# Kernel tuning notes

Measured on AMD Instinct MI355X. Metric: run time of the kernel, lower is better.

The kernel has to match this reference:

```python
import jax, jax.numpy as jnp
import numpy as np

VOCAB, EMBED, HIDDEN = 256, 512, 1024
B, T = 64, 512


def setup_inputs() -> dict:
    key = jax.random.key(0)
    ks = jax.random.split(key, 12)
    s = 0.02
    return {
        "x": jax.random.randint(ks[0], (B, T), 0, VOCAB),
        "embed": jax.random.normal(ks[1], (VOCAB, EMBED), jnp.float32) * s,
        "Wih0": jax.random.normal(ks[2], (3 * HIDDEN, EMBED), jnp.float32) * s,
        "Whh0": jax.random.normal(ks[3], (3 * HIDDEN, HIDDEN), jnp.float32) * s,
        "bih0": jax.random.normal(ks[4], (3 * HIDDEN,), jnp.float32) * s,
        "bhh0": jax.random.normal(ks[5], (3 * HIDDEN,), jnp.float32) * s,
        "Wih1": jax.random.normal(ks[6], (3 * HIDDEN, HIDDEN), jnp.float32) * s,
        "Whh1": jax.random.normal(ks[7], (3 * HIDDEN, HIDDEN), jnp.float32) * s,
        "bih1": jax.random.normal(ks[8], (3 * HIDDEN,), jnp.float32) * s,
        "bhh1": jax.random.normal(ks[9], (3 * HIDDEN,), jnp.float32) * s,
        "W_out": jax.random.normal(ks[10], (VOCAB, HIDDEN), jnp.float32) * s,
        "b_out": jax.random.normal(ks[11], (VOCAB,), jnp.float32) * s,
    }


def gru_cell(inp, h, Wih, Whh, bih, bhh):
    # PyTorch GRUCell math.
    gi = inp @ Wih.T + bih  # (B, 3H)
    gh = h @ Whh.T + bhh    # (B, 3H)
    i_r, i_z, i_n = jnp.split(gi, 3, axis=-1)
    h_r, h_z, h_n = jnp.split(gh, 3, axis=-1)
    r = jax.nn.sigmoid(i_r + h_r)
    z = jax.nn.sigmoid(i_z + h_z)
    n = jnp.tanh(i_n + r * h_n)
    return (1.0 - z) * n + z * h


def reference(x, embed, Wih0, Whh0, bih0, bhh0, Wih1, Whh1, bih1, bhh1, W_out, b_out):
    emb = embed[x]                       # (B, T, E)
    xs = jnp.swapaxes(emb, 0, 1)         # (T, B, E)
    h0 = jnp.zeros((x.shape[0], HIDDEN), emb.dtype)

    def step(carry, inp_t):
        h_0, h_1 = carry
        h_0 = gru_cell(inp_t, h_0, Wih0, Whh0, bih0, bhh0)
        h_1 = gru_cell(h_0, h_1, Wih1, Whh1, bih1, bhh1)
        return (h_0, h_1), h_1

    _, outs = jax.lax.scan(step, (h0, h0), xs)   # outs: (T, B, H)
    outs = jnp.swapaxes(outs, 0, 1)              # (B, T, H)
    logits = outs @ W_out.T + b_out              # (B, T, V)
    return logits
```

## Files before the change

kernel.cpp:

```cpp
#include <hip/hip_runtime.h>
#include <stdint.h>

typedef short short8 __attribute__((ext_vector_type(8)));
typedef float f32x4 __attribute__((ext_vector_type(4)));
typedef unsigned short u16;
typedef unsigned long long u64;

#define MFMA16(a, b, c) __builtin_amdgcn_mfma_f32_16x16x32_bf16((a), (b), (c), 0, 0, 0)

#define T_LEN 512
#define BATCH 64
#define EMB_D 512
#define HID 1024
#define VOC 256
#define NWG 256
#define THREADS 128
#define R0 256
#define R1 8
#define SLOT (BATCH * HID)

#define OFF_XT    0u
#define OFF_EMBT  131072u
#define OFF_WIH0  524288u
#define OFF_WHH0  3670016u
#define OFF_WIH1  9961472u
#define OFF_WHH1  16252928u
#define OFF_WOUT  22544384u
#define OFF_H0R   23068672u
#define OFF_H1R   56623104u
#define OFF_H1ALL 57671680u
#define OFF_SYNC  124780544u
#define SYNC_BYTES 65536u
#define WS_TOTAL  (OFF_SYNC + SYNC_BYTES)

static __device__ __forceinline__ u16 f2b(float f) {
  uint32_t u = __float_as_uint(f);
  u += 0x7FFFu + ((u >> 16) & 1u);
  return (u16)(u >> 16);
}
static __device__ __forceinline__ float sigm(float x) { return 1.0f / (1.0f + __expf(-x)); }

__global__ void cvt_kernel(const float* __restrict__ src, u16* __restrict__ dst, int n) {
  int i = ((int)blockIdx.x * 256 + (int)threadIdx.x) * 4;
  if (i + 4 <= n) {
    const float4 v = *(const float4*)(src + i);
    ushort4 o;
    o.x = f2b(v.x); o.y = f2b(v.y); o.z = f2b(v.z); o.w = f2b(v.w);
    *(ushort4*)(dst + i) = o;
  }
}

__global__ void xt_kernel(const int* __restrict__ x, int* __restrict__ xT) {
  const int t = (int)blockIdx.x, b = (int)threadIdx.x;
  xT[t * BATCH + b] = x[b * T_LEN + t];
}

__global__ __launch_bounds__(THREADS, 1) void rnn_persist_kernel(
    const int* __restrict__ xT, const u16* __restrict__ embtab,
    const u16* __restrict__ A0i_r, const u16* __restrict__ A0i_z, const u16* __restrict__ A0i_n,
    const u16* __restrict__ A0h_r, const u16* __restrict__ A0h_z, const u16* __restrict__ A0h_n,
    const u16* __restrict__ A1i_r, const u16* __restrict__ A1i_z, const u16* __restrict__ A1i_n,
    const u16* __restrict__ A1h_r, const u16* __restrict__ A1h_z, const u16* __restrict__ A1h_n,
    const float* __restrict__ bih0, const float* __restrict__ bhh0,
    const float* __restrict__ bih1, const float* __restrict__ bhh1,
    u16* __restrict__ h0r, u16* __restrict__ h1r,
    u16* __restrict__ h1all, unsigned* __restrict__ sync)
{
  const int tid = (int)threadIdx.x;
  const int wv = tid >> 6;
  const int lane = tid & 63;
  const int lrow = lane & 15;
  const int lk8 = (lane >> 4) << 3;
  const int bb = (int)blockIdx.x >> 6;
  const int g = (int)blockIdx.x & 63;
  const int layer = g >> 5;
  const int ub = g & 31;

  unsigned* p0 = sync;
  unsigned* p1 = sync + 4 * 64 * 32;
  const int widx = ub * 2 + wv;
  unsigned* myflag = (layer ? p1 : p0) + (size_t)(bb * 64 + widx) * 32;
  unsigned* pollf0 = p0 + (size_t)(bb * 64 + lane) * 32;
  unsigned* pollf1 = p1 + (size_t)(bb * 64 + lane) * 32;

  const u16 *Axr, *Axz, *Axn, *Ahr, *Ahz, *Ahn;
  int ldx;
  if (layer == 0) { Axr = A0i_r; Axz = A0i_z; Axn = A0i_n;
                    Ahr = A0h_r; Ahz = A0h_z; Ahn = A0h_n; ldx = EMB_D; }
  else            { Axr = A1i_r; Axz = A1i_z; Axn = A1i_n;
                    Ahr = A1h_r; Ahz = A1h_z; Ahn = A1h_n; ldx = HID; }
  const int urow = ub * 32 + wv * 16 + lrow;
  const size_t axrow = (size_t)urow * ldx;
  const size_t ahrow = (size_t)urow * HID;
  const int brow = bb * 16 + lrow;

  const float* bi = layer ? bih1 : bih0;
  const float* bh = layer ? bhh1 : bhh0;
  const int ubase_l = ub * 32 + wv * 16 + (lane >> 4) * 4;
  const int batch = bb * 16 + (lane & 15);
  float bR[4], bZ[4], bNi[4], bNh[4], hp[4];
#pragma unroll
  for (int r = 0; r < 4; ++r) {
    const int ug = ubase_l + r;
    bR[r] = bi[ug] + bh[ug];
    bZ[r] = bi[HID + ug] + bh[HID + ug];
    bNi[r] = bi[2 * HID + ug];
    bNh[r] = bh[2 * HID + ug];
    hp[r] = 0.f;
  }
  const size_t hoff = (size_t)batch * HID + ubase_l;

  const int sBeg = layer ? 1 : 0;
  const int sEnd = layer ? T_LEN : (T_LEN - 1);

  for (int s = sBeg; s <= sEnd; ++s) {
    {
      const unsigned t0 = (unsigned)s;
      unsigned v = __hip_atomic_load(pollf0, __ATOMIC_RELAXED, __HIP_MEMORY_SCOPE_AGENT);
      while (v < t0) { __builtin_amdgcn_s_sleep(1);
        v = __hip_atomic_load(pollf0, __ATOMIC_RELAXED, __HIP_MEMORY_SCOPE_AGENT); }
    }
    if (layer) {
      const unsigned t1 = (unsigned)(s - 1);
      unsigned v = __hip_atomic_load(pollf1, __ATOMIC_RELAXED, __HIP_MEMORY_SCOPE_AGENT);
      while (v < t1) { __builtin_amdgcn_s_sleep(1);
        v = __hip_atomic_load(pollf1, __ATOMIC_RELAXED, __HIP_MEMORY_SCOPE_AGENT); }
    } else if (s >= 252) {
      const unsigned t1 = (unsigned)(s - 250);
      unsigned v = __hip_atomic_load(pollf1, __ATOMIC_RELAXED, __HIP_MEMORY_SCOPE_AGENT);
      while (v < t1) { __builtin_amdgcn_s_sleep(1);
        v = __hip_atomic_load(pollf1, __ATOMIC_RELAXED, __HIP_MEMORY_SCOPE_AGENT); }
    }

    const u16* h0p = h0r + (size_t)((s - 1) & (R0 - 1)) * SLOT;
    const u16* h1p = h1r + (size_t)((s - 2) & (R1 - 1)) * SLOT;

    f32x4 aR = {0.f, 0.f, 0.f, 0.f}, aZ = aR, aNi = aR, aNh = aR;

    if (layer == 0) {
      const int tok = xT[s * BATCH + brow];
      const u16* Bx = embtab + (size_t)tok * EMB_D;
#pragma unroll 8
      for (int ks = 0; ks < 16; ++ks) {
        const int kk = ks * 32 + lk8;
        const short8 ar = *(const short8*)(Axr + axrow + kk);
        const short8 az = *(const short8*)(Axz + axrow + kk);
        const short8 an = *(const short8*)(Axn + axrow + kk);
        const short8 bf = *(const short8*)(Bx + kk);
        aR = MFMA16(ar, bf, aR);
        aZ = MFMA16(az, bf, aZ);
        aNi = MFMA16(an, bf, aNi);
      }
    } else {
      const u16* Bx = h0p + (size_t)brow * HID;
#pragma unroll 8
      for (int ks = 0; ks < 32; ++ks) {
        const int kk = ks * 32 + lk8;
        const short8 ar = *(const short8*)(Axr + axrow + kk);
        const short8 az = *(const short8*)(Axz + axrow + kk);
        const short8 an = *(const short8*)(Axn + axrow + kk);
        const short8 bf = *(const short8*)(Bx + kk);
        aR = MFMA16(ar, bf, aR);
        aZ = MFMA16(az, bf, aZ);
        aNi = MFMA16(an, bf, aNi);
      }
    }
    {
      const u16* Bh = (layer ? h1p : h0p) + (size_t)brow * HID;
#pragma unroll 8
      for (int ks = 0; ks < 32; ++ks) {
        const int kk = ks * 32 + lk8;
        const short8 ar = *(const short8*)(Ahr + ahrow + kk);
        const short8 az = *(const short8*)(Ahz + ahrow + kk);
        const short8 an = *(const short8*)(Ahn + ahrow + kk);
        const short8 bf = *(const short8*)(Bh + kk);
        aR = MFMA16(ar, bf, aR);
        aZ = MFMA16(az, bf, aZ);
        aNh = MFMA16(an, bf, aNh);
      }
    }
    u16 hv0, hv1, hv2, hv3;
#pragma unroll
    for (int r = 0; r < 4; ++r) {
      const float rg = sigm(aR[r] + bR[r]);
      const float zg = sigm(aZ[r] + bZ[r]);
      const float ng = tanhf(aNi[r] + bNi[r] + rg * (aNh[r] + bNh[r]));
      const float hn = (1.0f - zg) * ng + zg * hp[r];
      hp[r] = hn;
      const u16 hv = f2b(hn);
      if (r == 0) hv0 = hv; else if (r == 1) hv1 = hv;
      else if (r == 2) hv2 = hv; else hv3 = hv;
    }
    const u64 packed = (u64)hv0 | ((u64)hv1 << 16) | ((u64)hv2 << 32) | ((u64)hv3 << 48);
    u16* wslot = layer ? (h1r + (size_t)((s - 1) & (R1 - 1)) * SLOT)
                       : (h0r + (size_t)(s & (R0 - 1)) * SLOT);
    __hip_atomic_store((u64*)(wslot + hoff), packed,
                       __ATOMIC_RELAXED, __HIP_MEMORY_SCOPE_AGENT);
    if (layer)
      *(u64*)(h1all + ((size_t)(s - 1) * BATCH + batch) * HID + ubase_l) = packed;

    asm volatile("s_waitcnt vmcnt(0)" ::: "memory");
    if (lane == 0)
      __hip_atomic_store(myflag, (unsigned)(layer ? s : s + 1),
                         __ATOMIC_RELAXED, __HIP_MEMORY_SCOPE_AGENT);
  }
}

__global__ __launch_bounds__(256, 2) void logits_kernel(
    const u16* __restrict__ h1all, const u16* __restrict__ Woutb,
    const float* __restrict__ bout, float* __restrict__ out)
{
  __shared__ __align__(16) short lds[16 * 4 * 64 * 8];
  const int tid = (int)threadIdx.x;
  const int wv = tid >> 6, lane = tid & 63;
  const int lrow = lane & 15, lk8 = (lane >> 4) << 3;
  const int row0 = (int)blockIdx.x * 64 + wv * 16;
  f32x4 acc[16];
#pragma unroll
  for (int i = 0; i < 16; ++i) acc[i] = (f32x4){0.f, 0.f, 0.f, 0.f};

  for (int kc = 0; kc < HID; kc += 128) {
    __syncthreads();
#pragma unroll
    for (int j = 0; j < 16; ++j) {
      const int slot = tid + j * 256;
      const int ct = slot >> 8, kt = (slot >> 6) & 3, l = slot & 63;
      *(short8*)&lds[slot * 8] =
          *(const short8*)(Woutb + (size_t)(ct * 16 + (l & 15)) * HID + kc + kt * 32 + ((l >> 4) << 3));
    }
    __syncthreads();
#pragma unroll
    for (int kt = 0; kt < 4; ++kt) {
      const short8 af = *(const short8*)(h1all + (size_t)(row0 + lrow) * HID + kc + kt * 32 + lk8);
#pragma unroll
      for (int ct = 0; ct < 16; ++ct) {
        const short8 bf = *(const short8*)&lds[((ct * 4 + kt) * 64 + lane) * 8];
        acc[ct] = MFMA16(af, bf, acc[ct]);
      }
    }
  }
#pragma unroll
  for (int ct = 0; ct < 16; ++ct) {
    const int v = ct * 16 + lrow;
    const float bo = bout[v];
#pragma unroll
    for (int r = 0; r < 4; ++r) {
      const int row = row0 + (lane >> 4) * 4 + r;
      const int t = row >> 6, b = row & 63;
      out[((size_t)(b * T_LEN + t)) * VOC + v] = acc[ct][r] + bo;
    }
  }
}

extern "C" void kernel_launch(void* const* d_in, const int* in_sizes, int n_in,
                              void* d_out, int out_size, void* d_ws, size_t ws_size,
                              hipStream_t stream) {
  const int*   x     = (const int*)d_in[0];
  const float* embed = (const float*)d_in[1];
  const float* Wih0  = (const float*)d_in[2];
  const float* Whh0  = (const float*)d_in[3];
  const float* bih0  = (const float*)d_in[4];
  const float* bhh0  = (const float*)d_in[5];
  const float* Wih1  = (const float*)d_in[6];
  const float* Whh1  = (const float*)d_in[7];
  const float* bih1  = (const float*)d_in[8];
  const float* bhh1  = (const float*)d_in[9];
  const float* Wout  = (const float*)d_in[10];
  const float* bout  = (const float*)d_in[11];
  float* out = (float*)d_out;
  char* ws = (char*)d_ws;
  if (ws_size < (size_t)WS_TOTAL) return;

  hipMemsetAsync(ws + OFF_H0R + (size_t)(R0 - 1) * SLOT * 2, 0, SLOT * 2, stream);
  hipMemsetAsync(ws + OFF_H1R + (size_t)(R1 - 1) * SLOT * 2, 0, SLOT * 2, stream);
  hipMemsetAsync(ws + OFF_SYNC, 0, SYNC_BYTES, stream);
  xt_kernel<<<512, 64, 0, stream>>>(x, (int*)(ws + OFF_XT));
  cvt_kernel<<<128, 256, 0, stream>>>(embed, (u16*)(ws + OFF_EMBT), 256 * 512);
  cvt_kernel<<<1536, 256, 0, stream>>>(Wih0, (u16*)(ws + OFF_WIH0), 3072 * 512);
  cvt_kernel<<<3072, 256, 0, stream>>>(Whh0, (u16*)(ws + OFF_WHH0), 3072 * 1024);
  cvt_kernel<<<3072, 256, 0, stream>>>(Wih1, (u16*)(ws + OFF_WIH1), 3072 * 1024);
  cvt_kernel<<<3072, 256, 0, stream>>>(Whh1, (u16*)(ws + OFF_WHH1), 3072 * 1024);
  cvt_kernel<<<256, 256, 0, stream>>>(Wout, (u16*)(ws + OFF_WOUT), 256 * 1024);

  const u16* wih0b = (const u16*)(ws + OFF_WIH0);
  const u16* whh0b = (const u16*)(ws + OFF_WHH0);
  const u16* wih1b = (const u16*)(ws + OFF_WIH1);
  const u16* whh1b = (const u16*)(ws + OFF_WHH1);

  rnn_persist_kernel<<<NWG, THREADS, 0, stream>>>(
      (const int*)(ws + OFF_XT), (const u16*)(ws + OFF_EMBT),
      wih0b, wih0b + 524288, wih0b + 1048576,
      whh0b, whh0b + 1048576, whh0b + 2097152,
      wih1b, wih1b + 1048576, wih1b + 2097152,
      whh1b, whh1b + 1048576, whh1b + 2097152,
      bih0, bhh0, bih1, bhh1,
      (u16*)(ws + OFF_H0R), (u16*)(ws + OFF_H1R),
      (u16*)(ws + OFF_H1ALL), (unsigned*)(ws + OFF_SYNC));

  logits_kernel<<<512, 256, 0, stream>>>((const u16*)(ws + OFF_H1ALL),
                                         (const u16*)(ws + OFF_WOUT), bout, out);
}
```

Measured before the change: 9.401 ms.

## Split persistent GRU kernel into one-wave workgroups and use wave-wide flag polling

```diff
diff --git a/kernel.cpp b/kernel.cpp
--- a/kernel.cpp
+++ b/kernel.cpp
@@ -13,8 +13,6 @@
 #define EMB_D 512
 #define HID 1024
 #define VOC 256
-#define NWG 256
-#define THREADS 128
 #define R0 256
 #define R1 8
 #define SLOT (BATCH * HID)
@@ -40,6 +38,15 @@
 }
 static __device__ __forceinline__ float sigm(float x) { return 1.0f / (1.0f + __expf(-x)); }
 
+static __device__ __forceinline__ void wpoll(unsigned* base, unsigned tgt) {
+  unsigned* f = base + (size_t)(threadIdx.x & 63) * 32;
+  for (;;) {
+    const unsigned v = __hip_atomic_load(f, __ATOMIC_RELAXED, __HIP_MEMORY_SCOPE_AGENT);
+    if (__all((int)(v >= tgt))) break;
+    __builtin_amdgcn_s_sleep(1);
+  }
+}
+
 __global__ void cvt_kernel(const float* __restrict__ src, u16* __restrict__ dst, int n) {
   int i = ((int)blockIdx.x * 256 + (int)threadIdx.x) * 4;
   if (i + 4 <= n) {
@@ -55,7 +62,7 @@
   xT[t * BATCH + b] = x[b * T_LEN + t];
 }
 
-__global__ __launch_bounds__(THREADS, 1) void rnn_persist_kernel(
+__global__ __launch_bounds__(64, 1) void rnn_persist_kernel(
     const int* __restrict__ xT, const u16* __restrict__ embtab,
     const u16* __restrict__ A0i_r, const u16* __restrict__ A0i_z, const u16* __restrict__ A0i_n,
     const u16* __restrict__ A0h_r, const u16* __restrict__ A0h_z, const u16* __restrict__ A0h_n,
@@ -66,22 +73,19 @@
     u16* __restrict__ h0r, u16* __restrict__ h1r,
     u16* __restrict__ h1all, unsigned* __restrict__ sync)
 {
-  const int tid = (int)threadIdx.x;
-  const int wv = tid >> 6;
-  const int lane = tid & 63;
+  const int lane = (int)threadIdx.x;
   const int lrow = lane & 15;
   const int lk8 = (lane >> 4) << 3;
-  const int bb = (int)blockIdx.x >> 6;
-  const int g = (int)blockIdx.x & 63;
-  const int layer = g >> 5;
-  const int ub = g & 31;
-
-  unsigned* p0 = sync;
-  unsigned* p1 = sync + 4 * 64 * 32;
-  const int widx = ub * 2 + wv;
-  unsigned* myflag = (layer ? p1 : p0) + (size_t)(bb * 64 + widx) * 32;
-  unsigned* pollf0 = p0 + (size_t)(bb * 64 + lane) * 32;
-  unsigned* pollf1 = p1 + (size_t)(bb * 64 + lane) * 32;
+  const int wgid = (int)blockIdx.x;
+  const int bt = wgid >> 7;
+  const int layer = (wgid >> 6) & 1;
+  const int ug = wgid & 63;
+
+  unsigned* f0 = sync;
+  unsigned* f1 = sync + 4 * 64 * 32;
+  unsigned* f0d = f0 + (size_t)(bt * 64) * 32;
+  unsigned* f1d = f1 + (size_t)(bt * 64) * 32;
+  unsigned* myflag = (layer ? f1d : f0d) + (size_t)ug * 32;
 
   const u16 *Axr, *Axz, *Axn, *Ahr, *Ahz, *Ahn;
   int ldx;
@@ -89,58 +93,45 @@
                     Ahr = A0h_r; Ahz = A0h_z; Ahn = A0h_n; ldx = EMB_D; }
   else            { Axr = A1i_r; Axz = A1i_z; Axn = A1i_n;
                     Ahr = A1h_r; Ahz = A1h_z; Ahn = A1h_n; ldx = HID; }
-  const int urow = ub * 32 + wv * 16 + lrow;
+  const int urow = ug * 16 + lrow;
   const size_t axrow = (size_t)urow * ldx;
   const size_t ahrow = (size_t)urow * HID;
-  const int brow = bb * 16 + lrow;
+  const int brow = bt * 16 + lrow;
 
   const float* bi = layer ? bih1 : bih0;
   const float* bh = layer ? bhh1 : bhh0;
-  const int ubase_l = ub * 32 + wv * 16 + (lane >> 4) * 4;
-  const int batch = bb * 16 + (lane & 15);
+  const int ub4 = (lane >> 4) * 4;
+  const int eu0 = ug * 16 + ub4;
+  const int eb = bt * 16 + lrow;
   float bR[4], bZ[4], bNi[4], bNh[4], hp[4];
 #pragma unroll
   for (int r = 0; r < 4; ++r) {
-    const int ug = ubase_l + r;
-    bR[r] = bi[ug] + bh[ug];
-    bZ[r] = bi[HID + ug] + bh[HID + ug];
-    bNi[r] = bi[2 * HID + ug];
-    bNh[r] = bh[2 * HID + ug];
+    const int ugl = eu0 + r;
+    bR[r] = bi[ugl] + bh[ugl];
+    bZ[r] = bi[HID + ugl] + bh[HID + ugl];
+    bNi[r] = bi[2 * HID + ugl];
+    bNh[r] = bh[2 * HID + ugl];
     hp[r] = 0.f;
   }
-  const size_t hoff = (size_t)batch * HID + ubase_l;
+  const size_t hoff = (size_t)eb * HID + eu0;
 
   const int sBeg = layer ? 1 : 0;
   const int sEnd = layer ? T_LEN : (T_LEN - 1);
 
   for (int s = sBeg; s <= sEnd; ++s) {
-    {
-      const unsigned t0 = (unsigned)s;
-      unsigned v = __hip_atomic_load(pollf0, __ATOMIC_RELAXED, __HIP_MEMORY_SCOPE_AGENT);
-      while (v < t0) { __builtin_amdgcn_s_sleep(1);
-        v = __hip_atomic_load(pollf0, __ATOMIC_RELAXED, __HIP_MEMORY_SCOPE_AGENT); }
-    }
-    if (layer) {
-      const unsigned t1 = (unsigned)(s - 1);
-      unsigned v = __hip_atomic_load(pollf1, __ATOMIC_RELAXED, __HIP_MEMORY_SCOPE_AGENT);
-      while (v < t1) { __builtin_amdgcn_s_sleep(1);
-        v = __hip_atomic_load(pollf1, __ATOMIC_RELAXED, __HIP_MEMORY_SCOPE_AGENT); }
-    } else if (s >= 252) {
-      const unsigned t1 = (unsigned)(s - 250);
-      unsigned v = __hip_atomic_load(pollf1, __ATOMIC_RELAXED, __HIP_MEMORY_SCOPE_AGENT);
-      while (v < t1) { __builtin_amdgcn_s_sleep(1);
-        v = __hip_atomic_load(pollf1, __ATOMIC_RELAXED, __HIP_MEMORY_SCOPE_AGENT); }
-    }
-
-    const u16* h0p = h0r + (size_t)((s - 1) & (R0 - 1)) * SLOT;
-    const u16* h1p = h1r + (size_t)((s - 2) & (R1 - 1)) * SLOT;
+    wpoll(f0d, (unsigned)s);
+    if (layer) wpoll(f1d, (unsigned)(s - 1));
+    else if (s >= 252) wpoll(f1d, (unsigned)(s - 250));
+
+    const u16* h0prev = h0r + (size_t)((s - 1) & (R0 - 1)) * SLOT;
+    const u16* h1prev = h1r + (size_t)((s - 2) & (R1 - 1)) * SLOT;
 
     f32x4 aR = {0.f, 0.f, 0.f, 0.f}, aZ = aR, aNi = aR, aNh = aR;
 
     if (layer == 0) {
       const int tok = xT[s * BATCH + brow];
       const u16* Bx = embtab + (size_t)tok * EMB_D;
-#pragma unroll 8
+#pragma unroll 4
       for (int ks = 0; ks < 16; ++ks) {
         const int kk = ks * 32 + lk8;
         const short8 ar = *(const short8*)(Axr + axrow + kk);
@@ -151,9 +142,21 @@
         aZ = MFMA16(az, bf, aZ);
         aNi = MFMA16(an, bf, aNi);
       }
+      const u16* Bh = h0prev + (size_t)brow * HID;
+#pragma unroll 4
+      for (int ks = 0; ks < 32; ++ks) {
+        const int kk = ks * 32 + lk8;
+        const short8 ar = *(const short8*)(Ahr + ahrow + kk);
+        const short8 az = *(const short8*)(Ahz + ahrow + kk);
+        const short8 an = *(const short8*)(Ahn + ahrow + kk);
+        const short8 bf = *(const short8*)(Bh + kk);
+        aR = MFMA16(ar, bf, aR);
+        aZ = MFMA16(az, bf, aZ);
+        aNh = MFMA16(an, bf, aNh);
+      }
     } else {
-      const u16* Bx = h0p + (size_t)brow * HID;
-#pragma unroll 8
+      const u16* Bx = h0prev + (size_t)brow * HID;
+#pragma unroll 4
       for (int ks = 0; ks < 32; ++ks) {
         const int kk = ks * 32 + lk8;
         const short8 ar = *(const short8*)(Axr + axrow + kk);
@@ -164,10 +167,8 @@
         aZ = MFMA16(az, bf, aZ);
         aNi = MFMA16(an, bf, aNi);
       }
-    }
-    {
-      const u16* Bh = (layer ? h1p : h0p) + (size_t)brow * HID;
-#pragma unroll 8
+      const u16* Bh = h1prev + (size_t)brow * HID;
+#pragma unroll 4
       for (int ks = 0; ks < 32; ++ks) {
         const int kk = ks * 32 + lk8;
         const short8 ar = *(const short8*)(Ahr + ahrow + kk);
@@ -179,7 +180,8 @@
         aNh = MFMA16(an, bf, aNh);
       }
     }
-    u16 hv0, hv1, hv2, hv3;
+
+    u16 hv[4];
 #pragma unroll
     for (int r = 0; r < 4; ++r) {
       const float rg = sigm(aR[r] + bR[r]);
@@ -187,22 +189,21 @@
       const float ng = tanhf(aNi[r] + bNi[r] + rg * (aNh[r] + bNh[r]));
       const float hn = (1.0f - zg) * ng + zg * hp[r];
       hp[r] = hn;
-      const u16 hv = f2b(hn);
-      if (r == 0) hv0 = hv; else if (r == 1) hv1 = hv;
-      else if (r == 2) hv2 = hv; else hv3 = hv;
-    }
-    const u64 packed = (u64)hv0 | ((u64)hv1 << 16) | ((u64)hv2 << 32) | ((u64)hv3 << 48);
+      hv[r] = f2b(hn);
+    }
+    const u64 packed = (u64)hv[0] | ((u64)hv[1] << 16) | ((u64)hv[2] << 32) | ((u64)hv[3] << 48);
     u16* wslot = layer ? (h1r + (size_t)((s - 1) & (R1 - 1)) * SLOT)
                        : (h0r + (size_t)(s & (R0 - 1)) * SLOT);
     __hip_atomic_store((u64*)(wslot + hoff), packed,
                        __ATOMIC_RELAXED, __HIP_MEMORY_SCOPE_AGENT);
-    if (layer)
-      *(u64*)(h1all + ((size_t)(s - 1) * BATCH + batch) * HID + ubase_l) = packed;
 
     asm volatile("s_waitcnt vmcnt(0)" ::: "memory");
     if (lane == 0)
       __hip_atomic_store(myflag, (unsigned)(layer ? s : s + 1),
                          __ATOMIC_RELAXED, __HIP_MEMORY_SCOPE_AGENT);
+    if (layer)
+      __hip_atomic_store((u64*)(h1all + ((size_t)(s - 1) * BATCH + eb) * HID + eu0),
+                         packed, __ATOMIC_RELAXED, __HIP_MEMORY_SCOPE_AGENT);
   }
 }
 
@@ -287,7 +288,7 @@
   const u16* wih1b = (const u16*)(ws + OFF_WIH1);
   const u16* whh1b = (const u16*)(ws + OFF_WHH1);
 
-  rnn_persist_kernel<<<NWG, THREADS, 0, stream>>>(
+  rnn_persist_kernel<<<512, 64, 0, stream>>>(
       (const int*)(ws + OFF_XT), (const u16*)(ws + OFF_EMBT),
       wih0b, wih0b + 524288, wih0b + 1048576,
       whh0b, whh0b + 1048576, whh0b + 2097152,
```

Result: no change. 9.549 ms (+1.6%).
